# Optimization experiments

Measured on AMD Instinct MI355X. Metric: run time of the kernel, lower is better.

## Reference

```python
import jax, jax.numpy as jnp
import numpy as np

NUM_BLOCKS = 4
BLOCK_SIZE = 2048
BATCH = 512
NUM_ITERATIONS = 2
# static tridiagonal block sparsity pattern: (out_block_i, in_block_j)
BLOCK_PAIRS = [(0, 0), (0, 1), (1, 0), (1, 1), (1, 2), (2, 1), (2, 2), (2, 3), (3, 2), (3, 3)]


def setup_inputs() -> dict:
    key = jax.random.key(0)
    kx, kw, kb = jax.random.split(key, 3)
    X = jax.random.normal(kx, (NUM_BLOCKS, BATCH, BLOCK_SIZE), dtype=jnp.float32)
    # torch nn.Linear default init: U(-1/sqrt(fan_in), 1/sqrt(fan_in))
    bound = 1.0 / np.sqrt(BLOCK_SIZE)
    W = jax.random.uniform(kw, (len(BLOCK_PAIRS), BLOCK_SIZE, BLOCK_SIZE),
                           minval=-bound, maxval=bound, dtype=jnp.float32)
    b = jax.random.uniform(kb, (len(BLOCK_PAIRS), BLOCK_SIZE),
                           minval=-bound, maxval=bound, dtype=jnp.float32)
    return {"X": X, "W": W, "b": b}


def reference(X, W, b):
    # X: [num_blocks, batch, block_size]
    # W: [n_present_blocks, out_feat, in_feat], b: [n_present_blocks, out_feat]
    # Each iteration: y_i = relu( sum_{j : (i,j) present} x_j @ W_ij^T + b_ij )
    for _ in range(NUM_ITERATIONS):
        Y = jnp.zeros_like(X)
        for k, (i, j) in enumerate(BLOCK_PAIRS):  # small static set of block GEMMs
            Y = Y.at[i].add(jnp.einsum('be,oe->bo', X[j], W[k]) + b[k])
        X = jax.nn.relu(Y)
    return X
```

## Files before the change

### kernel.cpp

```cpp
#include <hip/hip_runtime.h>
#include <cstdint>
#include <cstddef>

typedef __bf16 bf16;
typedef bf16 bf16x4 __attribute__((ext_vector_type(4)));
typedef bf16 bf16x8 __attribute__((ext_vector_type(8)));
typedef float f32x4 __attribute__((ext_vector_type(4)));

#define NB 4
#define BATCH 512
#define BS 2048
#define NPAIRS 10
#define KQ 4
#define KSPAN (BS / KQ)

__constant__ int c_npairs[NB] = {2, 3, 3, 2};
__constant__ int c_pj[NB][3]  = {{0, 1, 0}, {0, 1, 2}, {1, 2, 3}, {2, 3, 0}};
__constant__ int c_pk[NB][3]  = {{0, 1, 0}, {2, 3, 4}, {5, 6, 7}, {8, 9, 0}};

__global__ __launch_bounds__(256) void cvt_kernel(
    const float* __restrict__ X, const float* __restrict__ W,
    const float* __restrict__ b,
    bf16* __restrict__ Xbf, bf16* __restrict__ Wbf, float* __restrict__ bias4)
{
    const int nW4 = NPAIRS * BS * BS / 4;
    const int nX4 = NB * BATCH * BS / 4;
    int idx    = blockIdx.x * 256 + threadIdx.x;
    int stride = 8192 * 256;
    const float4* W4 = (const float4*)W;
    const float4* X4 = (const float4*)X;
    for (int i = idx; i < nW4; i += stride) {
        float4 v = W4[i];
        bf16x4 o = { (bf16)v.x, (bf16)v.y, (bf16)v.z, (bf16)v.w };
        *(bf16x4*)(Wbf + 4 * (size_t)i) = o;
    }
    if (idx < nX4) {
        float4 v = X4[idx];
        bf16x4 o = { (bf16)v.x, (bf16)v.y, (bf16)v.z, (bf16)v.w };
        *(bf16x4*)(Xbf + 4 * (size_t)idx) = o;
    }
    if (idx < NB * BS) {
        int i = idx >> 11;
        int o2 = idx & (BS - 1);
        float s = 0.f;
        int np = c_npairs[i];
        for (int p = 0; p < np; ++p) s += b[c_pk[i][p] * BS + o2];
        bias4[idx] = s;
    }
}

typedef __attribute__((address_space(1))) void void_g;
typedef __attribute__((address_space(3))) void void_l;

__device__ __forceinline__ void gload16(const bf16* g, bf16* l)
{
    __builtin_amdgcn_global_load_lds((void_g*)g, (void_l*)l, 16, 0, 0);
}

__global__ __launch_bounds__(256, 4) void gemm_ksplit(
    const bf16* __restrict__ Xbf,
    const bf16* __restrict__ Wbf,
    float* __restrict__ P)
{
    __shared__ bf16 sA[128 * 32];
    __shared__ bf16 sB[128 * 32];

    const int tid  = threadIdx.x;
    const int lane = tid & 63;
    const int wid  = tid >> 6;
    const int wm   = (wid & 1) * 64;
    const int wn   = (wid >> 1) * 64;
    const int z    = blockIdx.z;
    const int ib   = z >> 2;
    const int kq   = z & 3;
    const int bm0  = blockIdx.y * 128;
    const int bn0  = blockIdx.x * 128;

    f32x4 acc[4][4];
    const f32x4 zero = {0.f, 0.f, 0.f, 0.f};
#pragma unroll
    for (int i = 0; i < 4; ++i)
#pragma unroll
        for (int j = 0; j < 4; ++j) acc[i][j] = zero;

    const int srow = tid >> 2;
    const int skp  = (tid & 3) * 8;
    bf16* ldsA0 = sA + (size_t)tid * 8;
    bf16* ldsA1 = sA + 2048 + (size_t)tid * 8;
    bf16* ldsB0 = sB + (size_t)tid * 8;
    bf16* ldsB1 = sB + 2048 + (size_t)tid * 8;

    const int lm = lane & 15;
    const int lk = (lane >> 4) * 8;

    const int np = c_npairs[ib];
    for (int p = 0; p < np; ++p) {
        const bf16* Ab = Xbf + ((size_t)c_pj[ib][p] * BATCH + bm0 + srow) * BS
                             + kq * KSPAN + skp;
        const bf16* Bb = Wbf + ((size_t)c_pk[ib][p] * BS    + bn0 + srow) * BS
                             + kq * KSPAN + skp;
        for (int k0 = 0; k0 < KSPAN; k0 += 32) {
            __syncthreads();
            gload16(Ab + k0,            ldsA0);
            gload16(Ab + 64 * BS + k0,  ldsA1);
            gload16(Bb + k0,            ldsB0);
            gload16(Bb + 64 * BS + k0,  ldsB1);
            __syncthreads();

            bf16x8 af[4], bfr[4];
#pragma unroll
            for (int mi = 0; mi < 4; ++mi)
                af[mi] = *(const bf16x8*)(sA + (wm + mi * 16 + lm) * 32 + lk);
#pragma unroll
            for (int ni = 0; ni < 4; ++ni)
                bfr[ni] = *(const bf16x8*)(sB + (wn + ni * 16 + lm) * 32 + lk);
#pragma unroll
            for (int mi = 0; mi < 4; ++mi)
#pragma unroll
                for (int ni = 0; ni < 4; ++ni)
                    acc[mi][ni] = __builtin_amdgcn_mfma_f32_16x16x32_bf16(
                        af[mi], bfr[ni], acc[mi][ni], 0, 0, 0);
        }
    }

    float* Pt = P + ((size_t)z * BATCH + bm0) * BS + bn0;
#pragma unroll
    for (int mi = 0; mi < 4; ++mi) {
#pragma unroll
        for (int ni = 0; ni < 4; ++ni) {
            const int m = wm + mi * 16 + (lane >> 4) * 4;
            const int n = wn + ni * 16 + lm;
#pragma unroll
            for (int r = 0; r < 4; ++r)
                Pt[(size_t)(m + r) * BS + n] = acc[mi][ni][r];
        }
    }
}

__global__ __launch_bounds__(256) void combine_kernel(
    const float* __restrict__ P, const float* __restrict__ bias4,
    bf16* __restrict__ Xnext, float* __restrict__ Yout, int write_f32)
{
    const int e4 = blockIdx.x * 256 + threadIdx.x;
    const int ib  = e4 >> 18;
    const int loc = e4 & 262143;
    const float4* Pb = (const float4*)P + (size_t)(ib * KQ) * 262144 + loc;
    float4 p0 = Pb[0];
    float4 p1 = Pb[262144];
    float4 p2 = Pb[2 * 262144];
    float4 p3 = Pb[3 * 262144];
    const int n4 = e4 & 511;
    float4 bv = ((const float4*)bias4)[ib * 512 + n4];
    float sx = p0.x + p1.x + p2.x + p3.x + bv.x;
    float sy = p0.y + p1.y + p2.y + p3.y + bv.y;
    float sz = p0.z + p1.z + p2.z + p3.z + bv.z;
    float sw = p0.w + p1.w + p2.w + p3.w + bv.w;
    sx = sx > 0.f ? sx : 0.f;
    sy = sy > 0.f ? sy : 0.f;
    sz = sz > 0.f ? sz : 0.f;
    sw = sw > 0.f ? sw : 0.f;
    if (write_f32) {
        float4 o = { sx, sy, sz, sw };
        ((float4*)Yout)[e4] = o;
    } else {
        bf16x4 o = { (bf16)sx, (bf16)sy, (bf16)sz, (bf16)sw };
        *(bf16x4*)(Xnext + 4 * (size_t)e4) = o;
    }
}

extern "C" void kernel_launch(void* const* d_in, const int* in_sizes, int n_in,
                              void* d_out, int out_size, void* d_ws, size_t ws_size,
                              hipStream_t stream)
{
    const float* X = (const float*)d_in[0];
    const float* W = (const float*)d_in[1];
    const float* b = (const float*)d_in[2];
    float* out = (float*)d_out;
    char* ws = (char*)d_ws;

    const size_t W_BYTES   = (size_t)NPAIRS * BS * BS * 2;
    const size_t XBF_BYTES = (size_t)NB * BATCH * BS * 2;
    const size_t P_BYTES   = (size_t)NB * KQ * BATCH * BS * 4;

    bf16*  Wbf   = (bf16*)ws;
    bf16*  Xbf0  = (bf16*)(ws + W_BYTES);
    bf16*  Xbf1  = (bf16*)(ws + W_BYTES + XBF_BYTES);
    float* P     = (float*)(ws + W_BYTES + 2 * XBF_BYTES);
    float* bias4 = (float*)(ws + W_BYTES + 2 * XBF_BYTES + P_BYTES);

    hipLaunchKernelGGL(cvt_kernel, dim3(8192), dim3(256), 0, stream,
                       X, W, b, Xbf0, Wbf, bias4);

    dim3 grid(BS / 128, BATCH / 128, NB * KQ);
    hipLaunchKernelGGL(gemm_ksplit, grid, dim3(256), 0, stream, Xbf0, Wbf, P);
    hipLaunchKernelGGL(combine_kernel, dim3(4096), dim3(256), 0, stream,
                       P, bias4, Xbf1, (float*)nullptr, 0);
    hipLaunchKernelGGL(gemm_ksplit, grid, dim3(256), 0, stream, Xbf1, Wbf, P);
    hipLaunchKernelGGL(combine_kernel, dim3(4096), dim3(256), 0, stream,
                       P, bias4, (bf16*)nullptr, out, 1);
}
```

Baseline: 386.6 us.

## Double-buffer LDS tiles to overlap global loads with MFMA compute

```diff
diff --git a/kernel.cpp b/kernel.cpp
--- a/kernel.cpp
+++ b/kernel.cpp
@@ -62,8 +62,8 @@
     const bf16* __restrict__ Wbf,
     float* __restrict__ P)
 {
-    __shared__ bf16 sA[128 * 32];
-    __shared__ bf16 sB[128 * 32];
+    __shared__ bf16 sA[2][128 * 32];
+    __shared__ bf16 sB[2][128 * 32];
 
     const int tid  = threadIdx.x;
     const int lane = tid & 63;
@@ -75,6 +75,8 @@
     const int kq   = z & 3;
     const int bm0  = blockIdx.y * 128;
     const int bn0  = blockIdx.x * 128;
+    const int np     = c_npairs[ib];
+    const int nsteps = np * (KSPAN / 32);
 
     f32x4 acc[4][4];
     const f32x4 zero = {0.f, 0.f, 0.f, 0.f};
@@ -85,42 +87,50 @@
 
     const int srow = tid >> 2;
     const int skp  = (tid & 3) * 8;
-    bf16* ldsA0 = sA + (size_t)tid * 8;
-    bf16* ldsA1 = sA + 2048 + (size_t)tid * 8;
-    bf16* ldsB0 = sB + (size_t)tid * 8;
-    bf16* ldsB1 = sB + 2048 + (size_t)tid * 8;
+
+    const bf16* A_0 = Xbf + ((size_t)c_pj[ib][0] * BATCH + bm0 + srow) * BS + kq * KSPAN + skp;
+    const bf16* A_1 = Xbf + ((size_t)c_pj[ib][1] * BATCH + bm0 + srow) * BS + kq * KSPAN + skp;
+    const bf16* A_2 = Xbf + ((size_t)c_pj[ib][2] * BATCH + bm0 + srow) * BS + kq * KSPAN + skp;
+    const bf16* B_0 = Wbf + ((size_t)c_pk[ib][0] * BS + bn0 + srow) * BS + kq * KSPAN + skp;
+    const bf16* B_1 = Wbf + ((size_t)c_pk[ib][1] * BS + bn0 + srow) * BS + kq * KSPAN + skp;
+    const bf16* B_2 = Wbf + ((size_t)c_pk[ib][2] * BS + bn0 + srow) * BS + kq * KSPAN + skp;
 
     const int lm = lane & 15;
     const int lk = (lane >> 4) * 8;
 
-    const int np = c_npairs[ib];
-    for (int p = 0; p < np; ++p) {
-        const bf16* Ab = Xbf + ((size_t)c_pj[ib][p] * BATCH + bm0 + srow) * BS
-                             + kq * KSPAN + skp;
-        const bf16* Bb = Wbf + ((size_t)c_pk[ib][p] * BS    + bn0 + srow) * BS
-                             + kq * KSPAN + skp;
-        for (int k0 = 0; k0 < KSPAN; k0 += 32) {
-            __syncthreads();
-            gload16(Ab + k0,            ldsA0);
-            gload16(Ab + 64 * BS + k0,  ldsA1);
-            gload16(Bb + k0,            ldsB0);
-            gload16(Bb + 64 * BS + k0,  ldsB1);
-            __syncthreads();
-
-            bf16x8 af[4], bfr[4];
-#pragma unroll
-            for (int mi = 0; mi < 4; ++mi)
-                af[mi] = *(const bf16x8*)(sA + (wm + mi * 16 + lm) * 32 + lk);
+    auto stage = [&](int s, int buf) {
+        const int p  = s >> 4;
+        const int k0 = (s & 15) * 32;
+        const bf16* Ab = (p == 0) ? A_0 : ((p == 1) ? A_1 : A_2);
+        const bf16* Bb = (p == 0) ? B_0 : ((p == 1) ? B_1 : B_2);
+        bf16* la = &sA[buf][tid * 8];
+        bf16* lb = &sB[buf][tid * 8];
+        gload16(Ab + k0,           la);
+        gload16(Ab + 64 * BS + k0, la + 2048);
+        gload16(Bb + k0,           lb);
+        gload16(Bb + 64 * BS + k0, lb + 2048);
+    };
+
+    stage(0, 0);
+
+    for (int s = 0; s < nsteps; ++s) {
+        const int cur = s & 1;
+        __syncthreads();
+        if (s + 1 < nsteps) stage(s + 1, cur ^ 1);
+
+        bf16x8 af[4], bfr[4];
+#pragma unroll
+        for (int mi = 0; mi < 4; ++mi)
+            af[mi] = *(const bf16x8*)(&sA[cur][(wm + mi * 16 + lm) * 32 + lk]);
+#pragma unroll
+        for (int ni = 0; ni < 4; ++ni)
+            bfr[ni] = *(const bf16x8*)(&sB[cur][(wn + ni * 16 + lm) * 32 + lk]);
+#pragma unroll
+        for (int mi = 0; mi < 4; ++mi)
 #pragma unroll
             for (int ni = 0; ni < 4; ++ni)
-                bfr[ni] = *(const bf16x8*)(sB + (wn + ni * 16 + lm) * 32 + lk);
-#pragma unroll
-            for (int mi = 0; mi < 4; ++mi)
-#pragma unroll
-                for (int ni = 0; ni < 4; ++ni)
-                    acc[mi][ni] = __builtin_amdgcn_mfma_f32_16x16x32_bf16(
-                        af[mi], bfr[ni], acc[mi][ni], 0, 0, 0);
-        }
+                acc[mi][ni] = __builtin_amdgcn_mfma_f32_16x16x32_bf16(
+                    af[mi], bfr[ni], acc[mi][ni], 0, 0, 0);
     }
 
     float* Pt = P + ((size_t)z * BATCH + bm0) * BS + bn0;
```

Result: slower. 481.0 us (+24.4%).
